# Kernel tuning notes

Hardware: AMD Instinct MI355X
Metric: run time of the kernel (lower is better)

The kernel has to match this reference:

```python
import jax, jax.numpy as jnp
import numpy as np

B, S, HID, NH = 2, 2048, 2048, 16
NOPE, ROPE, VD = 128, 64, 128
QKD = NOPE + ROPE          # 192
KVR, QR = 512, 1536
EPS = 1e-6
SCALE = QKD ** (-0.5)


def rmsnorm(x, gamma, eps=EPS):
    return x * jax.lax.rsqrt(jnp.mean(x * x, axis=-1, keepdims=True) + eps) * gamma


def rotate_half(x):
    h = x.shape[-1] // 2
    return jnp.concatenate([-x[..., h:], x[..., :h]], axis=-1)


def apply_rope(x, cos, sin):
    # x: [b, h, s, d_rope]; cos/sin: [b, 1, s, d_rope]
    return x * cos + rotate_half(x) * sin


def setup_inputs() -> dict:
    key = jax.random.key(0)
    ks = jax.random.split(key, 8)
    hidden_states = jax.random.normal(ks[0], (B, S, HID), dtype=jnp.float32)
    # Standard NeoX-style rotary tables for the decoupled RoPE sub-dim
    pos = jnp.arange(S, dtype=jnp.float32)
    inv_freq = 1.0 / (10000.0 ** (jnp.arange(0, ROPE, 2, dtype=jnp.float32) / ROPE))
    freqs = pos[:, None] * inv_freq[None, :]              # [S, ROPE/2]
    emb = jnp.concatenate([freqs, freqs], axis=-1)        # [S, ROPE]
    cos = jnp.broadcast_to(jnp.cos(emb)[None], (B, S, ROPE)).astype(jnp.float32)
    sin = jnp.broadcast_to(jnp.sin(emb)[None], (B, S, ROPE)).astype(jnp.float32)
    std = 0.02
    Wq_down = jax.random.normal(ks[1], (QR, HID), dtype=jnp.float32) * std
    q_gamma = jnp.ones((QR,), dtype=jnp.float32)
    Wq_up = jax.random.normal(ks[2], (NH * QKD, QR), dtype=jnp.float32) * std
    Wkv_down = jax.random.normal(ks[3], (KVR + ROPE, HID), dtype=jnp.float32) * std
    kv_gamma = jnp.ones((KVR,), dtype=jnp.float32)
    Wkv_up = jax.random.normal(ks[4], (NH * (NOPE + VD), KVR), dtype=jnp.float32) * std
    Wo = jax.random.normal(ks[5], (HID, NH * VD), dtype=jnp.float32) * std
    return {
        "hidden_states": hidden_states, "cos": cos, "sin": sin,
        "Wq_down": Wq_down, "q_gamma": q_gamma, "Wq_up": Wq_up,
        "Wkv_down": Wkv_down, "kv_gamma": kv_gamma, "Wkv_up": Wkv_up,
        "Wo": Wo,
    }


def reference(hidden_states, cos, sin, Wq_down, q_gamma, Wq_up,
              Wkv_down, kv_gamma, Wkv_up, Wo):
    b, s, _ = hidden_states.shape
    cos4 = cos[:, None, :, :]  # [b,1,s,ROPE]
    sin4 = sin[:, None, :, :]

    # Q path: low-rank down -> RMSNorm -> up
    q_lat = rmsnorm(hidden_states @ Wq_down.T, q_gamma)            # [b,s,QR]
    q = (q_lat @ Wq_up.T).reshape(b, s, NH, QKD).transpose(0, 2, 1, 3)  # [b,h,s,QKD]
    q_nope, q_rope = q[..., :NOPE], q[..., NOPE:]
    q_rope = apply_rope(q_rope, cos4, sin4)
    q = jnp.concatenate([q_nope, q_rope], axis=-1)                 # [b,h,s,QKD]

    # KV path: joint down-proj -> split latent / shared rope key
    kv = hidden_states @ Wkv_down.T                                # [b,s,KVR+ROPE]
    c_kv, k_rope = kv[..., :KVR], kv[..., KVR:]
    c_kv = rmsnorm(c_kv, kv_gamma)
    kvx = (c_kv @ Wkv_up.T).reshape(b, s, NH, NOPE + VD).transpose(0, 2, 1, 3)
    k_nope, v = kvx[..., :NOPE], kvx[..., NOPE:]                   # [b,h,s,*]

    # Shared rope key, broadcast to all heads, rotated
    k_rope = apply_rope(k_rope[:, None, :, :], cos4, sin4)         # [b,1,s,ROPE]
    k_rope = jnp.broadcast_to(k_rope, (b, NH, s, ROPE))
    k = jnp.concatenate([k_nope, k_rope], axis=-1)                 # [b,h,s,QKD]

    # SDPA with causal mask (V zero-padded to QKD in the original -> identical
    # to using V directly and slicing, so we use V directly)
    scores = jnp.einsum('bhqd,bhkd->bhqk', q, k) * SCALE           # [b,h,s,s]
    causal = jnp.tril(jnp.ones((s, s), dtype=bool))
    scores = jnp.where(causal[None, None], scores, jnp.finfo(scores.dtype).min)
    attn = jax.nn.softmax(scores, axis=-1)
    out = jnp.einsum('bhqk,bhkd->bhqd', attn, v)                   # [b,h,s,VD]
    out = out.transpose(0, 2, 1, 3).reshape(b, s, NH * VD)
    return out @ Wo.T                                              # [b,s,HID]
```

## Files before the change

### kernel.cpp

```cpp
#include <hip/hip_runtime.h>
#include <math.h>

#define SCALE_F 0.0721687836487032f

typedef __attribute__((ext_vector_type(8))) short bf16x8;
typedef __attribute__((ext_vector_type(4))) float f32x4;
typedef __attribute__((ext_vector_type(4))) unsigned short u16x4;

static __device__ __forceinline__ short f2bf(float f) {
  unsigned u = __float_as_uint(f);
  u += 0x7fffu + ((u >> 16) & 1u);
  return (short)(u >> 16);
}

static __device__ __forceinline__ void gl_lds16(const void* g, void* l) {
  __builtin_amdgcn_global_load_lds((const __attribute__((address_space(1))) void*)g,
                                   (__attribute__((address_space(3))) void*)l, 16, 0, 0);
}

template <int MODE>
__global__ __launch_bounds__(256) void gemm_mfma(
    const short* __restrict__ A, const short* __restrict__ W,
    void* __restrict__ Cout, int N, int K,
    const float* __restrict__ cosb, const float* __restrict__ sinb,
    short* __restrict__ out2)
{
  __shared__ __align__(16) short As[128 * 32];
  __shared__ __align__(16) short Ws[128 * 32];
  const int tid = threadIdx.x;
  const int lane = tid & 63;
  const int quad = lane >> 4, n16 = lane & 15;
  const int bm = blockIdx.y * 128, bn = blockIdx.x * 128;
  const int wr = ((tid >> 6) >> 1) * 64, wc = ((tid >> 6) & 1) * 64;

  f32x4 acc[4][4];
  #pragma unroll
  for (int i = 0; i < 4; ++i)
    #pragma unroll
    for (int j = 0; j < 4; ++j) acc[i][j] = (f32x4){0.f, 0.f, 0.f, 0.f};

  const int r0 = tid >> 2, c0 = (tid & 3) * 8;
  const short* a0p = A + (size_t)(bm + r0) * K + c0;
  const short* a1p = A + (size_t)(bm + 64 + r0) * K + c0;
  const short* w0p = W + (size_t)(bn + r0) * K + c0;
  const short* w1p = W + (size_t)(bn + 64 + r0) * K + c0;
  short* asd0 = &As[tid * 8];
  short* asd1 = &As[2048 + tid * 8];
  short* wsd0 = &Ws[tid * 8];
  short* wsd1 = &Ws[2048 + tid * 8];

  for (int k0 = 0; k0 < K; k0 += 32) {
    gl_lds16(a0p, asd0);
    gl_lds16(a1p, asd1);
    gl_lds16(w0p, wsd0);
    gl_lds16(w1p, wsd1);
    a0p += 32; a1p += 32; w0p += 32; w1p += 32;
    __syncthreads();

    bf16x8 af[4], wf[4];
    #pragma unroll
    for (int i = 0; i < 4; ++i) {
      af[i] = *(const bf16x8*)&As[(wr + i * 16 + n16) * 32 + quad * 8];
      wf[i] = *(const bf16x8*)&Ws[(wc + i * 16 + n16) * 32 + quad * 8];
    }
    #pragma unroll
    for (int i = 0; i < 4; ++i)
      #pragma unroll
      for (int j = 0; j < 4; ++j)
        acc[i][j] = __builtin_amdgcn_mfma_f32_16x16x32_bf16(af[i], wf[j], acc[i][j], 0, 0, 0);
    __syncthreads();
  }

  if (MODE == 0) {
    #pragma unroll
    for (int i = 0; i < 4; ++i)
      #pragma unroll
      for (int r = 0; r < 4; ++r) {
        size_t row = (size_t)(bm + wr + i * 16 + quad * 4 + r);
        #pragma unroll
        for (int j = 0; j < 4; ++j)
          ((float*)Cout)[row * N + bn + wc + j * 16 + n16] = acc[i][j][r];
      }
  } else if (MODE == 2) {
    #pragma unroll
    for (int i = 0; i < 4; ++i)
      #pragma unroll
      for (int r = 0; r < 4; ++r) {
        int m = bm + wr + i * 16 + quad * 4 + r;
        int bb = m >> 11, s = m & 2047;
        #pragma unroll
        for (int j = 0; j < 4; ++j) {
          int col = bn + wc + j * 16 + n16;
          int h = col / 192, c = col - h * 192;
          float v = acc[i][j][r];
          if (c >= 128) {
            int jr = c - 128;
            float part = acc[i][j ^ 2][r];
            float cs = cosb[(size_t)m * 64 + jr], sn = sinb[(size_t)m * 64 + jr];
            v = (jr < 32) ? (v * cs - part * sn) : (v * cs + part * sn);
          }
          ((short*)Cout)[(((size_t)(bb * 16 + h)) * 2048 + s) * 192 + c] = f2bf(v * SCALE_F);
        }
      }
  } else if (MODE == 3) {
    #pragma unroll
    for (int i = 0; i < 4; ++i)
      #pragma unroll
      for (int r = 0; r < 4; ++r) {
        int m = bm + wr + i * 16 + quad * 4 + r;
        int bb = m >> 11, s = m & 2047;
        #pragma unroll
        for (int j = 0; j < 4; ++j) {
          int col = bn + wc + j * 16 + n16;
          int h = col >> 8, c = col & 255;
          short v = f2bf(acc[i][j][r]);
          if (c < 128)
            ((short*)Cout)[(((size_t)(bb * 16 + h)) * 2048 + s) * 192 + c] = v;
          else
            out2[((size_t)(bb * 16 + h) * 128 + (c - 128)) * 2048 + s] = v;
        }
      }
    if ((bn & 255) == 0) {
      const short* kr = (const short*)sinb;
      const int h = bn >> 8;
      const int bb = bm >> 11, sb = bm & 2047;
      const int rr = tid >> 1, half = tid & 1;
      const short* src = kr + (size_t)(bm + rr) * 64 + half * 32;
      short* dst = (short*)Cout + (((size_t)(bb * 16 + h)) * 2048 + sb + rr) * 192 + 128 + half * 32;
      #pragma unroll
      for (int k = 0; k < 4; ++k)
        *(bf16x8*)(dst + k * 8) = *(const bf16x8*)(src + k * 8);
    }
  } else {
    float* qlat = (float*)Cout;
    float* kvf  = (float*)out2;
    #pragma unroll
    for (int i = 0; i < 4; ++i)
      #pragma unroll
      for (int r = 0; r < 4; ++r) {
        size_t row = (size_t)(bm + wr + i * 16 + quad * 4 + r);
        #pragma unroll
        for (int j = 0; j < 4; ++j) {
          int col = bn + wc + j * 16 + n16;
          if (col < 1536) qlat[row * 1536 + col] = acc[i][j][r];
          else            kvf[row * 640 + (col - 1536)] = acc[i][j][r];
        }
      }
  }
}

__global__ __launch_bounds__(256) void cast_all(
    const float* __restrict__ hidden, const float* __restrict__ Wqd,
    const float* __restrict__ Wqu, const float* __restrict__ Wkvu,
    const float* __restrict__ Wo, const float* __restrict__ Wkvd,
    short* __restrict__ hb, short* __restrict__ Wqd_b, short* __restrict__ Wqu_b,
    short* __restrict__ Wkvu_b, short* __restrict__ Wo_b, short* __restrict__ Wkvd_b)
{
  int blk = blockIdx.x;
  const float* src; short* dst; int i;
  if (blk < 8192)       { src = hidden; dst = hb;     i = (blk * 256 + threadIdx.x) * 4; }
  else if (blk < 11264) { src = Wqd;  dst = Wqd_b;  i = ((blk - 8192) * 256 + threadIdx.x) * 4; }
  else if (blk < 15872) { src = Wqu;  dst = Wqu_b;  i = ((blk - 11264) * 256 + threadIdx.x) * 4; }
  else if (blk < 17920) { src = Wkvu; dst = Wkvu_b; i = ((blk - 15872) * 256 + threadIdx.x) * 4; }
  else if (blk < 22016) { src = Wo;   dst = Wo_b;   i = ((blk - 17920) * 256 + threadIdx.x) * 4; }
  else {
    i = ((blk - 22016) * 256 + threadIdx.x) * 4;
    int r = i >> 11;
    short4 o = {0, 0, 0, 0};
    if (r < 576) {
      float4 v = *(const float4*)(Wkvd + i);
      o.x = f2bf(v.x); o.y = f2bf(v.y); o.z = f2bf(v.z); o.w = f2bf(v.w);
    }
    *(short4*)(Wkvd_b + i) = o;
    return;
  }
  float4 v = *(const float4*)(src + i);
  short4 o = { f2bf(v.x), f2bf(v.y), f2bf(v.z), f2bf(v.w) };
  *(short4*)(dst + i) = o;
}

__global__ __launch_bounds__(256) void rmsnorm_both(
    const float* __restrict__ q_lat, const float* __restrict__ q_gamma,
    short* __restrict__ q_lat_b,
    const float* __restrict__ kvf, const float* __restrict__ kv_gamma,
    const float* __restrict__ cosb, const float* __restrict__ sinb,
    short* __restrict__ ckv, short* __restrict__ kr)
{
  const int tid = threadIdx.x;
  __shared__ float red[4];
  if (blockIdx.x < 4096) {
    const int m = blockIdx.x;
    const float* x = q_lat + (size_t)m * 1536;
    short* y = q_lat_b + (size_t)m * 1536;
    float ss = 0.f;
    for (int c = tid * 4; c < 1536; c += 1024) {
      float4 v = *(const float4*)(x + c);
      ss += v.x * v.x + v.y * v.y + v.z * v.z + v.w * v.w;
    }
    #pragma unroll
    for (int off = 32; off > 0; off >>= 1) ss += __shfl_down(ss, off, 64);
    if ((tid & 63) == 0) red[tid >> 6] = ss;
    __syncthreads();
    float tot = red[0] + red[1] + red[2] + red[3];
    float scale = rsqrtf(tot / 1536.f + 1e-6f);
    for (int c = tid * 4; c < 1536; c += 1024) {
      float4 v = *(const float4*)(x + c);
      float4 g = *(const float4*)(q_gamma + c);
      short4 o = { f2bf(v.x * scale * g.x), f2bf(v.y * scale * g.y),
                   f2bf(v.z * scale * g.z), f2bf(v.w * scale * g.w) };
      *(short4*)(y + c) = o;
    }
  } else {
    const int m = blockIdx.x - 4096;
    const float* x = kvf + (size_t)m * 640;
    short* y = ckv + (size_t)m * 512;
    float ss = 0.f;
    for (int c = tid * 4; c < 512; c += 1024) {
      float4 v = *(const float4*)(x + c);
      ss += v.x * v.x + v.y * v.y + v.z * v.z + v.w * v.w;
    }
    #pragma unroll
    for (int off = 32; off > 0; off >>= 1) ss += __shfl_down(ss, off, 64);
    if ((tid & 63) == 0) red[tid >> 6] = ss;
    __syncthreads();
    float tot = red[0] + red[1] + red[2] + red[3];
    float scale = rsqrtf(tot / 512.f + 1e-6f);
    for (int c = tid * 4; c < 512; c += 1024) {
      float4 v = *(const float4*)(x + c);
      float4 g = *(const float4*)(kv_gamma + c);
      short4 o = { f2bf(v.x * scale * g.x), f2bf(v.y * scale * g.y),
                   f2bf(v.z * scale * g.z), f2bf(v.w * scale * g.w) };
      *(short4*)(y + c) = o;
    }
    if (tid < 32) {
      const float* cb = cosb + (size_t)m * 64;
      const float* sb = sinb + (size_t)m * 64;
      float x1 = x[512 + tid], x2 = x[512 + tid + 32];
      kr[(size_t)m * 64 + tid]      = f2bf(x1 * cb[tid] - x2 * sb[tid]);
      kr[(size_t)m * 64 + tid + 32] = f2bf(x2 * cb[tid + 32] + x1 * sb[tid + 32]);
    }
  }
}

#define PSTR 72

__global__ __launch_bounds__(512) void flash_mfma(
    const short* __restrict__ Qb, const short* __restrict__ Kb,
    const short* __restrict__ Vt, short* __restrict__ attnb)
{
  __shared__ __align__(16) short KVs[2][40 * 512];
  __shared__ __align__(16) short Ps[8][32 * PSTR];

  const int h = blockIdx.x;
  const int p = blockIdx.y;
  const int b = blockIdx.z;
  const int bh = b * 16 + h;
  const int tid = threadIdx.x;
  const int wave = tid >> 6, lane = tid & 63;
  const int grp = wave >> 2, w4 = wave & 3;
  const int quad = lane >> 4, n16 = lane & 15;
  const int lq = lane >> 2, lr = lane & 3;
  const int qt_h = 15 - p;
  const int L = 2 * p + 2;
  const int NIT = 17;

  int qw = (grp ? p : qt_h) * 128 + w4 * 32;

  const short* kS[6]; short* kD[6];
  #pragma unroll
  for (int u = 0; u < 6; ++u) {
    kS[u] = Kb + ((size_t)bh * 2048 + w4 * 16 + lq) * 192 + u * 32 + lr * 8;
    kD[u] = &KVs[grp][(w4 * 6 + u) * 512 + lane * 8];
  }
  const short* vS[4]; short* vD[4];
  #pragma unroll
  for (int u = 0; u < 4; ++u) {
    int ci = w4 * 4 + u, ks = ci >> 3, vt = ci & 7;
    vS[u] = Vt + ((size_t)bh * 128 + vt * 16 + lq) * 2048 + ks * 32 + lr * 8;
    vD[u] = &KVs[grp][(24 + ci) * 512 + lane * 8];
  }

  bf16x8 aQ[2][6];
  #pragma unroll
  for (int rg = 0; rg < 2; ++rg) {
    const short* qp = Qb + ((size_t)bh * 2048 + qw + rg * 16 + n16) * 192 + quad * 8;
    #pragma unroll
    for (int t = 0; t < 6; ++t) aQ[rg][t] = *(const bf16x8*)(qp + t * 32);
  }

  f32x4 O[2][8];
  #pragma unroll
  for (int rg = 0; rg < 2; ++rg)
    #pragma unroll
    for (int i = 0; i < 8; ++i) O[rg][i] = (f32x4){0.f, 0.f, 0.f, 0.f};
  float lp[2] = {0.f, 0.f};

  short* pw = &Ps[wave][0];

  {
    #pragma unroll
    for (int u = 0; u < 6; ++u) gl_lds16(kS[u], kD[u]);
    #pragma unroll
    for (int u = 0; u < 4; ++u) gl_lds16(vS[u], vD[u]);
  }

  for (int j = 0; j < NIT; ++j) {
    __syncthreads();

    if (grp == 1 && j == L) {
      #pragma unroll
      for (int rg = 0; rg < 2; ++rg) {
        float l = lp[rg];
        l += __shfl_xor(l, 16);
        l += __shfl_xor(l, 32);
        float inv_l[4];
        #pragma unroll
        for (int r = 0; r < 4; ++r) inv_l[r] = 1.f / __shfl(l, quad * 4 + r);
        #pragma unroll
        for (int vt = 0; vt < 8; ++vt)
          #pragma unroll
          for (int r = 0; r < 4; ++r) {
            size_t m = (size_t)b * 2048 + qw + rg * 16 + quad * 4 + r;
            attnb[(m * 16 + h) * 128 + vt * 16 + n16] = f2bf(O[rg][vt][r] * inv_l[r]);
          }
      }
      #pragma unroll
      for (int rg = 0; rg < 2; ++rg)
        #pragma unroll
        for (int i = 0; i < 8; ++i) O[rg][i] = (f32x4){0.f, 0.f, 0.f, 0.f};
      lp[0] = 0.f; lp[1] = 0.f;
      qw = qt_h * 128 + w4 * 32;
      #pragma unroll
      for (int rg = 0; rg < 2; ++rg) {
        const short* qp = Qb + ((size_t)bh * 2048 + qw + rg * 16 + n16) * 192 + quad * 8;
        #pragma unroll
        for (int t = 0; t < 6; ++t) aQ[rg][t] = *(const bf16x8*)(qp + t * 32);
      }
    }

    const int kt = (grp == 0) ? j : (j < L ? j : 17 + j - L);

    if (kt * 64 <= qw + 31) {
      float s[4][2][4];
      bool act[4];
      const bool tail = (kt * 64 + 63 > qw);
      #pragma unroll
      for (int ct = 0; ct < 4; ++ct) {
        act[ct] = (kt * 64 + ct * 16 <= qw + 31);
        if (act[ct]) {
          f32x4 a0a = (f32x4){0.f, 0.f, 0.f, 0.f};
          f32x4 a1a = (f32x4){0.f, 0.f, 0.f, 0.f};
          f32x4 a0b = (f32x4){0.f, 0.f, 0.f, 0.f};
          f32x4 a1b = (f32x4){0.f, 0.f, 0.f, 0.f};
          #pragma unroll
          for (int t = 0; t < 3; ++t) {
            bf16x8 ak = *(const bf16x8*)&KVs[grp][(ct * 6 + t) * 512 + n16 * 32 + quad * 8];
            a0a = __builtin_amdgcn_mfma_f32_16x16x32_bf16(ak, aQ[0][t], a0a, 0, 0, 0);
            a1a = __builtin_amdgcn_mfma_f32_16x16x32_bf16(ak, aQ[1][t], a1a, 0, 0, 0);
          }
          #pragma unroll
          for (int t = 3; t < 6; ++t) {
            bf16x8 ak = *(const bf16x8*)&KVs[grp][(ct * 6 + t) * 512 + n16 * 32 + quad * 8];
            a0b = __builtin_amdgcn_mfma_f32_16x16x32_bf16(ak, aQ[0][t], a0b, 0, 0, 0);
            a1b = __builtin_amdgcn_mfma_f32_16x16x32_bf16(ak, aQ[1][t], a1b, 0, 0, 0);
          }
          #pragma unroll
          for (int r = 0; r < 4; ++r) {
            s[ct][0][r] = a0a[r] + a0b[r];
            s[ct][1][r] = a1a[r] + a1b[r];
          }
        }
      }

      #pragma unroll
      for (int rg = 0; rg < 2; ++rg) {
        const int q = qw + rg * 16 + n16;
        #pragma unroll
        for (int ct = 0; ct < 4; ++ct) {
          u16x4 pk;
          #pragma unroll
          for (int r = 0; r < 4; ++r) {
            float v = 0.f;
            if (act[ct]) {
              v = __expf(s[ct][rg][r]);
              if (tail) {
                int key = kt * 64 + ct * 16 + quad * 4 + r;
                if (key > q) v = 0.f;
              }
            }
            lp[rg] += v;
            pk[r] = (unsigned short)f2bf(v);
          }
          *(u16x4*)&pw[(rg * 16 + n16) * PSTR + ct * 16 + quad * 4] = pk;
        }
      }

      #pragma unroll
      for (int ks = 0; ks < 2; ++ks) {
        if (kt * 64 + ks * 32 <= qw + 31) {
          bf16x8 aP0 = *(const bf16x8*)&pw[(n16) * PSTR + ks * 32 + quad * 8];
          bf16x8 aP1 = *(const bf16x8*)&pw[(16 + n16) * PSTR + ks * 32 + quad * 8];
          #pragma unroll
          for (int vt = 0; vt < 8; ++vt) {
            bf16x8 bV = *(const bf16x8*)&KVs[grp][(24 + ks * 8 + vt) * 512 + n16 * 32 + quad * 8];
            O[0][vt] = __builtin_amdgcn_mfma_f32_16x16x32_bf16(aP0, bV, O[0][vt], 0, 0, 0);
            O[1][vt] = __builtin_amdgcn_mfma_f32_16x16x32_bf16(aP1, bV, O[1][vt], 0, 0, 0);
          }
        }
      }
    }

    __syncthreads();

    if (j + 1 < NIT) {
      const int jn = j + 1;
      const int ktn = (grp == 0) ? jn : (jn < L ? jn : 17 + jn - L);
      const size_t ka = (size_t)ktn * (64 * 192);
      const size_t va = (size_t)ktn * 64;
      #pragma unroll
      for (int u = 0; u < 6; ++u) gl_lds16(kS[u] + ka, kD[u]);
      #pragma unroll
      for (int u = 0; u < 4; ++u) gl_lds16(vS[u] + va, vD[u]);
    }
  }

  float* xO = (float*)&KVs[0][0];
  float* xl = (float*)&Ps[0][0];
  const int xb = w4 * 4160 + lane * 65;
  if (grp == 1) {
    #pragma unroll
    for (int rg = 0; rg < 2; ++rg)
      #pragma unroll
      for (int vt = 0; vt < 8; ++vt)
        #pragma unroll
        for (int r = 0; r < 4; ++r)
          xO[xb + rg * 32 + vt * 4 + r] = O[rg][vt][r];
    xl[w4 * 128 + lane * 2 + 0] = lp[0];
    xl[w4 * 128 + lane * 2 + 1] = lp[1];
  }
  __syncthreads();
  if (grp == 0) {
    #pragma unroll
    for (int rg = 0; rg < 2; ++rg)
      #pragma unroll
      for (int vt = 0; vt < 8; ++vt)
        #pragma unroll
        for (int r = 0; r < 4; ++r)
          O[rg][vt][r] += xO[xb + rg * 32 + vt * 4 + r];
    lp[0] += xl[w4 * 128 + lane * 2 + 0];
    lp[1] += xl[w4 * 128 + lane * 2 + 1];

    #pragma unroll
    for (int rg = 0; rg < 2; ++rg) {
      float l = lp[rg];
      l += __shfl_xor(l, 16);
      l += __shfl_xor(l, 32);
      float inv_l[4];
      #pragma unroll
      for (int r = 0; r < 4; ++r) inv_l[r] = 1.f / __shfl(l, quad * 4 + r);
      #pragma unroll
      for (int vt = 0; vt < 8; ++vt)
        #pragma unroll
        for (int r = 0; r < 4; ++r) {
          size_t m = (size_t)b * 2048 + qw + rg * 16 + quad * 4 + r;
          attnb[(m * 16 + h) * 128 + vt * 16 + n16] = f2bf(O[rg][vt][r] * inv_l[r]);
        }
    }
  }
}

extern "C" void kernel_launch(void* const* d_in, const int* in_sizes, int n_in,
                              void* d_out, int out_size, void* d_ws, size_t ws_size,
                              hipStream_t stream)
{
  const float* hidden   = (const float*)d_in[0];
  const float* cosb     = (const float*)d_in[1];
  const float* sinb     = (const float*)d_in[2];
  const float* Wq_down  = (const float*)d_in[3];
  const float* q_gamma  = (const float*)d_in[4];
  const float* Wq_up    = (const float*)d_in[5];
  const float* Wkv_down = (const float*)d_in[6];
  const float* kv_gamma = (const float*)d_in[7];
  const float* Wkv_up   = (const float*)d_in[8];
  const float* Wo       = (const float*)d_in[9];
  float* out = (float*)d_out;

  char* base = (char*)d_ws;
  short* hb  = (short*)base;
  float* kvf = (float*)(base + 16777216);
  short* Qb  = (short*)base;
  char* pB = base + 27262976;
  short* Wqd_b  = (short*)pB;
  short* Wkvd_b = (short*)(pB + 6291456);
  short* Wqu_b  = (short*)(pB + 8912896);
  short* Wkvu_b = (short*)(pB + 18350080);
  short* Wo_b   = (short*)(pB + 22544384);
  char* pC = pB + 30932992;
  float* q_lat = (float*)pC;
  short* Kb    = (short*)pC;
  char* pD = pC + 25165824;
  short* q_lat_b = (short*)pD;
  short* ckv_b   = (short*)(pD + 12582912);
  short* krope_b = (short*)(pD + 16777216);
  short* attn_b  = (short*)pD;
  char* pE = pD + 17301504;
  short* Vt = (short*)pE;

  dim3 blk(256);

  cast_all<<<23296, blk, 0, stream>>>(hidden, Wq_down, Wq_up, Wkv_up, Wo, Wkv_down,
                                      hb, Wqd_b, Wqu_b, Wkvu_b, Wo_b, Wkvd_b);

  gemm_mfma<4><<<dim3(17, 32), blk, 0, stream>>>(hb, Wqd_b, q_lat, 2176, 2048,
                                                 nullptr, nullptr, (short*)kvf);

  rmsnorm_both<<<8192, blk, 0, stream>>>(q_lat, q_gamma, q_lat_b,
                                         kvf, kv_gamma, cosb, sinb, ckv_b, krope_b);

  gemm_mfma<2><<<dim3(24, 32), blk, 0, stream>>>(q_lat_b, Wqu_b, Qb, 3072, 1536,
                                                 cosb, sinb, nullptr);
  gemm_mfma<3><<<dim3(32, 32), blk, 0, stream>>>(ckv_b, Wkvu_b, Kb, 4096, 512,
                                                 nullptr, (const float*)krope_b, Vt);

  flash_mfma<<<dim3(16, 8, 2), dim3(512), 0, stream>>>(Qb, Kb, Vt, attn_b);
  gemm_mfma<0><<<dim3(16, 32), blk, 0, stream>>>(attn_b, Wo_b, out, 2048, 2048,
                                                 nullptr, nullptr, nullptr);
}
```

Before: 479.1 us.

## Deepen GEMM K-tile to 64, merge Q/KV up-projections into one launch

The MFMA GEMM now loads a 64-wide K slab per barrier pair instead of 32, which halves the number of __syncthreads per K sweep at the cost of doubling LDS per block. The Q-up and KV-up GEMMs are fused into a single gemm_up launch that picks its operands by blockIdx, removing one kernel launch and letting both run concurrently on the GPU. The attention QK^T accumulation is also collapsed from two split accumulators back into one chain. That shortens code but serialises the MFMA dependency chain.

New measurement: 560.3 us. 1.17x slower.

```diff
diff --git a/kernel.cpp b/kernel.cpp
--- a/kernel.cpp
+++ b/kernel.cpp
@@ -25,13 +25,13 @@
     const float* __restrict__ cosb, const float* __restrict__ sinb,
     short* __restrict__ out2)
 {
-  __shared__ __align__(16) short As[128 * 32];
-  __shared__ __align__(16) short Ws[128 * 32];
+  __shared__ __align__(16) short As[2 * 128 * 32];
+  __shared__ __align__(16) short Ws[2 * 128 * 32];
   const int tid = threadIdx.x;
-  const int lane = tid & 63;
+  const int wv = tid >> 6, lane = tid & 63;
   const int quad = lane >> 4, n16 = lane & 15;
   const int bm = blockIdx.y * 128, bn = blockIdx.x * 128;
-  const int wr = ((tid >> 6) >> 1) * 64, wc = ((tid >> 6) & 1) * 64;
+  const int wr = (wv >> 1) * 64, wc = (wv & 1) * 64;
 
   f32x4 acc[4][4];
   #pragma unroll
@@ -39,35 +39,39 @@
     #pragma unroll
     for (int j = 0; j < 4; ++j) acc[i][j] = (f32x4){0.f, 0.f, 0.f, 0.f};
 
-  const int r0 = tid >> 2, c0 = (tid & 3) * 8;
-  const short* a0p = A + (size_t)(bm + r0) * K + c0;
-  const short* a1p = A + (size_t)(bm + 64 + r0) * K + c0;
-  const short* w0p = W + (size_t)(bn + r0) * K + c0;
-  const short* w1p = W + (size_t)(bn + 64 + r0) * K + c0;
-  short* asd0 = &As[tid * 8];
-  short* asd1 = &As[2048 + tid * 8];
-  short* wsd0 = &Ws[tid * 8];
-  short* wsd1 = &Ws[2048 + tid * 8];
-
-  for (int k0 = 0; k0 < K; k0 += 32) {
-    gl_lds16(a0p, asd0);
-    gl_lds16(a1p, asd1);
-    gl_lds16(w0p, wsd0);
-    gl_lds16(w1p, wsd1);
-    a0p += 32; a1p += 32; w0p += 32; w1p += 32;
-    __syncthreads();
-
-    bf16x8 af[4], wf[4];
+  const short* aS[4]; const short* wS[4]; short* aD[4]; short* wD[4];
+  #pragma unroll
+  for (int i = 0; i < 4; ++i) {
+    int c = wv * 4 + i, kk = c >> 3, rb = c & 7;
+    aS[i] = A + (size_t)(bm + rb * 16 + (lane >> 2)) * K + kk * 32 + (lane & 3) * 8;
+    wS[i] = W + (size_t)(bn + rb * 16 + (lane >> 2)) * K + kk * 32 + (lane & 3) * 8;
+    aD[i] = &As[c * 512 + lane * 8];
+    wD[i] = &Ws[c * 512 + lane * 8];
+  }
+
+  for (int k0 = 0; k0 < K; k0 += 64) {
     #pragma unroll
     for (int i = 0; i < 4; ++i) {
-      af[i] = *(const bf16x8*)&As[(wr + i * 16 + n16) * 32 + quad * 8];
-      wf[i] = *(const bf16x8*)&Ws[(wc + i * 16 + n16) * 32 + quad * 8];
-    }
-    #pragma unroll
-    for (int i = 0; i < 4; ++i)
-      #pragma unroll
-      for (int j = 0; j < 4; ++j)
-        acc[i][j] = __builtin_amdgcn_mfma_f32_16x16x32_bf16(af[i], wf[j], acc[i][j], 0, 0, 0);
+      gl_lds16(aS[i], aD[i]);
+      gl_lds16(wS[i], wD[i]);
+      aS[i] += 64; wS[i] += 64;
+    }
+    __syncthreads();
+
+    #pragma unroll
+    for (int kk = 0; kk < 2; ++kk) {
+      bf16x8 af[4], wf[4];
+      #pragma unroll
+      for (int i = 0; i < 4; ++i) {
+        af[i] = *(const bf16x8*)&As[kk * 4096 + (wr + i * 16 + n16) * 32 + quad * 8];
+        wf[i] = *(const bf16x8*)&Ws[kk * 4096 + (wc + i * 16 + n16) * 32 + quad * 8];
+      }
+      #pragma unroll
+      for (int i = 0; i < 4; ++i)
+        #pragma unroll
+        for (int j = 0; j < 4; ++j)
+          acc[i][j] = __builtin_amdgcn_mfma_f32_16x16x32_bf16(af[i], wf[j], acc[i][j], 0, 0, 0);
+    }
     __syncthreads();
   }
 
@@ -81,7 +85,90 @@
         for (int j = 0; j < 4; ++j)
           ((float*)Cout)[row * N + bn + wc + j * 16 + n16] = acc[i][j][r];
       }
-  } else if (MODE == 2) {
+  } else {
+    float* qlat = (float*)Cout;
+    float* kvf  = (float*)out2;
+    #pragma unroll
+    for (int i = 0; i < 4; ++i)
+      #pragma unroll
+      for (int r = 0; r < 4; ++r) {
+        size_t row = (size_t)(bm + wr + i * 16 + quad * 4 + r);
+        #pragma unroll
+        for (int j = 0; j < 4; ++j) {
+          int col = bn + wc + j * 16 + n16;
+          if (col < 1536) qlat[row * 1536 + col] = acc[i][j][r];
+          else            kvf[row * 640 + (col - 1536)] = acc[i][j][r];
+        }
+      }
+  }
+}
+
+__global__ __launch_bounds__(256) void gemm_up(
+    const short* __restrict__ Aq, const short* __restrict__ Wq,
+    short* __restrict__ Qb,
+    const float* __restrict__ cosb, const float* __restrict__ sinb,
+    const short* __restrict__ Akv, const short* __restrict__ Wkv,
+    short* __restrict__ Kb, short* __restrict__ Vtb,
+    const short* __restrict__ krope)
+{
+  __shared__ __align__(16) short As[2 * 128 * 32];
+  __shared__ __align__(16) short Ws[2 * 128 * 32];
+
+  const bool isQ = blockIdx.x < 24;
+  const short* A = isQ ? Aq : Akv;
+  const short* W = isQ ? Wq : Wkv;
+  const int K = isQ ? 1536 : 512;
+  const int bx = isQ ? blockIdx.x : (blockIdx.x - 24);
+
+  const int tid = threadIdx.x;
+  const int wv = tid >> 6, lane = tid & 63;
+  const int quad = lane >> 4, n16 = lane & 15;
+  const int bm = blockIdx.y * 128, bn = bx * 128;
+  const int wr = (wv >> 1) * 64, wc = (wv & 1) * 64;
+
+  f32x4 acc[4][4];
+  #pragma unroll
+  for (int i = 0; i < 4; ++i)
+    #pragma unroll
+    for (int j = 0; j < 4; ++j) acc[i][j] = (f32x4){0.f, 0.f, 0.f, 0.f};
+
+  const short* aS[4]; const short* wS[4]; short* aD[4]; short* wD[4];
+  #pragma unroll
+  for (int i = 0; i < 4; ++i) {
+    int c = wv * 4 + i, kk = c >> 3, rb = c & 7;
+    aS[i] = A + (size_t)(bm + rb * 16 + (lane >> 2)) * K + kk * 32 + (lane & 3) * 8;
+    wS[i] = W + (size_t)(bn + rb * 16 + (lane >> 2)) * K + kk * 32 + (lane & 3) * 8;
+    aD[i] = &As[c * 512 + lane * 8];
+    wD[i] = &Ws[c * 512 + lane * 8];
+  }
+
+  for (int k0 = 0; k0 < K; k0 += 64) {
+    #pragma unroll
+    for (int i = 0; i < 4; ++i) {
+      gl_lds16(aS[i], aD[i]);
+      gl_lds16(wS[i], wD[i]);
+      aS[i] += 64; wS[i] += 64;
+    }
+    __syncthreads();
+
+    #pragma unroll
+    for (int kk = 0; kk < 2; ++kk) {
+      bf16x8 af[4], wf[4];
+      #pragma unroll
+      for (int i = 0; i < 4; ++i) {
+        af[i] = *(const bf16x8*)&As[kk * 4096 + (wr + i * 16 + n16) * 32 + quad * 8];
+        wf[i] = *(const bf16x8*)&Ws[kk * 4096 + (wc + i * 16 + n16) * 32 + quad * 8];
+      }
+      #pragma unroll
+      for (int i = 0; i < 4; ++i)
+        #pragma unroll
+        for (int j = 0; j < 4; ++j)
+          acc[i][j] = __builtin_amdgcn_mfma_f32_16x16x32_bf16(af[i], wf[j], acc[i][j], 0, 0, 0);
+    }
+    __syncthreads();
+  }
+
+  if (isQ) {
     #pragma unroll
     for (int i = 0; i < 4; ++i)
       #pragma unroll
@@ -99,10 +186,10 @@
             float cs = cosb[(size_t)m * 64 + jr], sn = sinb[(size_t)m * 64 + jr];
             v = (jr < 32) ? (v * cs - part * sn) : (v * cs + part * sn);
           }
-          ((short*)Cout)[(((size_t)(bb * 16 + h)) * 2048 + s) * 192 + c] = f2bf(v * SCALE_F);
-        }
-      }
-  } else if (MODE == 3) {
+          Qb[(((size_t)(bb * 16 + h)) * 2048 + s) * 192 + c] = f2bf(v * SCALE_F);
+        }
+      }
+  } else {
     #pragma unroll
     for (int i = 0; i < 4; ++i)
       #pragma unroll
@@ -115,37 +202,21 @@
           int h = col >> 8, c = col & 255;
           short v = f2bf(acc[i][j][r]);
           if (c < 128)
-            ((short*)Cout)[(((size_t)(bb * 16 + h)) * 2048 + s) * 192 + c] = v;
+            Kb[(((size_t)(bb * 16 + h)) * 2048 + s) * 192 + c] = v;
           else
-            out2[((size_t)(bb * 16 + h) * 128 + (c - 128)) * 2048 + s] = v;
+            Vtb[((size_t)(bb * 16 + h) * 128 + (c - 128)) * 2048 + s] = v;
         }
       }
     if ((bn & 255) == 0) {
-      const short* kr = (const short*)sinb;
       const int h = bn >> 8;
       const int bb = bm >> 11, sb = bm & 2047;
       const int rr = tid >> 1, half = tid & 1;
-      const short* src = kr + (size_t)(bm + rr) * 64 + half * 32;
-      short* dst = (short*)Cout + (((size_t)(bb * 16 + h)) * 2048 + sb + rr) * 192 + 128 + half * 32;
+      const short* src = krope + (size_t)(bm + rr) * 64 + half * 32;
+      short* dst = Kb + (((size_t)(bb * 16 + h)) * 2048 + sb + rr) * 192 + 128 + half * 32;
       #pragma unroll
       for (int k = 0; k < 4; ++k)
         *(bf16x8*)(dst + k * 8) = *(const bf16x8*)(src + k * 8);
     }
-  } else {
-    float* qlat = (float*)Cout;
-    float* kvf  = (float*)out2;
-    #pragma unroll
-    for (int i = 0; i < 4; ++i)
-      #pragma unroll
-      for (int r = 0; r < 4; ++r) {
-        size_t row = (size_t)(bm + wr + i * 16 + quad * 4 + r);
-        #pragma unroll
-        for (int j = 0; j < 4; ++j) {
-          int col = bn + wc + j * 16 + n16;
-          if (col < 1536) qlat[row * 1536 + col] = acc[i][j][r];
-          else            kvf[row * 640 + (col - 1536)] = acc[i][j][r];
-        }
-      }
   }
 }
 
@@ -348,27 +419,16 @@
       for (int ct = 0; ct < 4; ++ct) {
         act[ct] = (kt * 64 + ct * 16 <= qw + 31);
         if (act[ct]) {
-          f32x4 a0a = (f32x4){0.f, 0.f, 0.f, 0.f};
-          f32x4 a1a = (f32x4){0.f, 0.f, 0.f, 0.f};
-          f32x4 a0b = (f32x4){0.f, 0.f, 0.f, 0.f};
-          f32x4 a1b = (f32x4){0.f, 0.f, 0.f, 0.f};
+          f32x4 a0 = (f32x4){0.f, 0.f, 0.f, 0.f};
+          f32x4 a1 = (f32x4){0.f, 0.f, 0.f, 0.f};
           #pragma unroll
-          for (int t = 0; t < 3; ++t) {
+          for (int t = 0; t < 6; ++t) {
             bf16x8 ak = *(const bf16x8*)&KVs[grp][(ct * 6 + t) * 512 + n16 * 32 + quad * 8];
-            a0a = __builtin_amdgcn_mfma_f32_16x16x32_bf16(ak, aQ[0][t], a0a, 0, 0, 0);
-            a1a = __builtin_amdgcn_mfma_f32_16x16x32_bf16(ak, aQ[1][t], a1a, 0, 0, 0);
+            a0 = __builtin_amdgcn_mfma_f32_16x16x32_bf16(ak, aQ[0][t], a0, 0, 0, 0);
+            a1 = __builtin_amdgcn_mfma_f32_16x16x32_bf16(ak, aQ[1][t], a1, 0, 0, 0);
           }
           #pragma unroll
-          for (int t = 3; t < 6; ++t) {
-            bf16x8 ak = *(const bf16x8*)&KVs[grp][(ct * 6 + t) * 512 + n16 * 32 + quad * 8];
-            a0b = __builtin_amdgcn_mfma_f32_16x16x32_bf16(ak, aQ[0][t], a0b, 0, 0, 0);
-            a1b = __builtin_amdgcn_mfma_f32_16x16x32_bf16(ak, aQ[1][t], a1b, 0, 0, 0);
-          }
-          #pragma unroll
-          for (int r = 0; r < 4; ++r) {
-            s[ct][0][r] = a0a[r] + a0b[r];
-            s[ct][1][r] = a1a[r] + a1b[r];
-          }
+          for (int r = 0; r < 4; ++r) { s[ct][0][r] = a0[r]; s[ct][1][r] = a1[r]; }
         }
       }
 
@@ -517,10 +577,8 @@
   rmsnorm_both<<<8192, blk, 0, stream>>>(q_lat, q_gamma, q_lat_b,
                                          kvf, kv_gamma, cosb, sinb, ckv_b, krope_b);
 
-  gemm_mfma<2><<<dim3(24, 32), blk, 0, stream>>>(q_lat_b, Wqu_b, Qb, 3072, 1536,
-                                                 cosb, sinb, nullptr);
-  gemm_mfma<3><<<dim3(32, 32), blk, 0, stream>>>(ckv_b, Wkvu_b, Kb, 4096, 512,
-                                                 nullptr, (const float*)krope_b, Vt);
+  gemm_up<<<dim3(56, 32), blk, 0, stream>>>(q_lat_b, Wqu_b, Qb, cosb, sinb,
+                                            ckv_b, Wkvu_b, Kb, Vt, krope_b);
 
   flash_mfma<<<dim3(16, 8, 2), dim3(512), 0, stream>>>(Qb, Kb, Vt, attn_b);
   gemm_mfma<0><<<dim3(16, 32), blk, 0, stream>>>(attn_b, Wo_b, out, 2048, 2048,
```
